# Optimization experiments

Hardware: AMD Instinct MI355X
Metric: run time of the kernel (lower is better)

## Reference

```python
import jax, jax.numpy as jnp
import numpy as np

H1, H, OUT, T = 512, 2048, 1024, 4096

def setup_inputs() -> dict:
    key = jax.random.key(0)
    ks = jax.random.split(key, 20)
    s = 0.02
    return {
        "input": jax.random.normal(ks[0], (1, OUT), jnp.float32),
        "hidden": jax.random.normal(ks[1], (1, 1, H), jnp.float32) * 0.1,
        "encoder_outputs": jax.random.normal(ks[2], (T, H), jnp.float32),
        "prenet_w": jax.random.normal(ks[3], (H1, OUT), jnp.float32) * s,
        "prenet_b": jnp.zeros((H1,), jnp.float32),
        "prenet2_w": jax.random.normal(ks[4], (H, H1), jnp.float32) * s,
        "prenet2_b": jnp.zeros((H,), jnp.float32),
        "attn1_w": jax.random.normal(ks[5], (H, H), jnp.float32) * s,
        "attn2_w": jax.random.normal(ks[6], (H, H), jnp.float32) * s,
        "attn3_w": jax.random.normal(ks[7], (1, H), jnp.float32) * s,
        "gru_w_ih": jax.random.normal(ks[8], (3 * H, 2 * H), jnp.float32) * s,
        "gru_w_hh": jax.random.normal(ks[9], (3 * H, H), jnp.float32) * s,
        "gru_b_ih": jnp.zeros((3 * H,), jnp.float32),
        "gru_b_hh": jnp.zeros((3 * H,), jnp.float32),
        "lin_w": jax.random.normal(ks[10], (OUT, H), jnp.float32) * s,
        "lin_b": jnp.zeros((OUT,), jnp.float32),
    }

def reference(input, hidden, encoder_outputs, prenet_w, prenet_b, prenet2_w,
              prenet2_b, attn1_w, attn2_w, attn3_w, gru_w_ih, gru_w_hh,
              gru_b_ih, gru_b_hh, lin_w, lin_b):
    # prenet MLP (dropout in eval mode = identity)
    em6 = jax.nn.relu(jax.nn.relu(input @ prenet_w.T + prenet_b) @ prenet2_w.T + prenet2_b)  # [1,H]
    # Bahdanau additive attention
    way = em6 @ attn1_w.T                                 # [1,H]
    uah = encoder_outputs @ attn2_w.T                     # [T,H]
    beta = jnp.tanh(way + uah)                            # [T,H] (broadcast = expand_as)
    gamma = beta @ attn3_w.T                              # [T,1]
    attn_weights = jax.nn.softmax(gamma.T, axis=1)        # [1,T]
    attn_applied = attn_weights @ encoder_outputs         # [1,H]
    # single-step GRU (PyTorch gate order: r, z, n)
    x = jnp.concatenate([em6, attn_applied], axis=1)      # [1,2H]
    h0 = hidden[0]                                        # [1,H]
    gi = x @ gru_w_ih.T + gru_b_ih                        # [1,3H]
    gh = h0 @ gru_w_hh.T + gru_b_hh                       # [1,3H]
    i_r, i_z, i_n = jnp.split(gi, 3, axis=1)
    h_r, h_z, h_n = jnp.split(gh, 3, axis=1)
    r = jax.nn.sigmoid(i_r + h_r)
    z = jax.nn.sigmoid(i_z + h_z)
    n = jnp.tanh(i_n + r * h_n)
    h_new = (1.0 - z) * n + z * h0                        # [1,H]
    out = jax.nn.softmax(h_new @ lin_w.T + lin_b, axis=1) # [1,OUT]
    return out, h_new[None], attn_weights
```

## Files before the change

### kernel.cpp

```cpp
#include <hip/hip_runtime.h>
#include <hip/hip_bf16.h>

typedef __bf16 bf16x8 __attribute__((ext_vector_type(8)));
typedef __bf16 bf16x4 __attribute__((ext_vector_type(4)));
typedef float f32x4 __attribute__((ext_vector_type(4)));

#define H1 512
#define H 2048
#define OUTN 1024
#define T 4096

__global__ __launch_bounds__(256) void matvec_k(
    const float* __restrict__ W, const float* __restrict__ x,
    const float* __restrict__ b, float* __restrict__ out,
    int R, int K, int relu)
{
    int row = blockIdx.x * 4 + (threadIdx.x >> 6);
    int lane = threadIdx.x & 63;
    if (row >= R) return;
    const float* Wr = W + (size_t)row * K;
    float s = 0.f;
    for (int k = lane * 4; k < K; k += 256) {
        float4 w4 = *(const float4*)(Wr + k);
        float4 x4 = *(const float4*)(x + k);
        s += w4.x * x4.x + w4.y * x4.y + w4.z * x4.z + w4.w * x4.w;
    }
    #pragma unroll
    for (int m = 32; m; m >>= 1) s += __shfl_xor(s, m, 64);
    if (lane == 0) {
        if (b) s += b[row];
        if (relu) s = fmaxf(s, 0.f);
        out[row] = s;
    }
}

__global__ __launch_bounds__(256) void cvt_frag_k(
    const float* __restrict__ E, const float* __restrict__ W2,
    __bf16* __restrict__ dst, float* __restrict__ zero_acc)
{
    if (blockIdx.x == 0) {
        #pragma unroll
        for (int j = 0; j < 8; ++j)
            zero_acc[threadIdx.x + 256 * j] = 0.f;
    }
    const int EC = T * H / 8;
    int c = blockIdx.x * 256 + threadIdx.x;
    const float* src;
    __bf16* d;
    if (c < EC) {
        int lane = c & 63;
        int k32 = (c >> 6) & 63;
        int r16 = c >> 12;
        int row = r16 * 16 + (lane & 15);
        int col = k32 * 32 + (lane >> 4) * 8;
        src = E + (size_t)row * H + col;
        d = dst + (size_t)c * 8;
    } else {
        int c2 = c - EC;
        int row = c2 >> 8;
        int kc = c2 & 255;
        src = W2 + (size_t)row * H + kc * 8;
        int grp = kc >> 3, cc = kc & 7;
        int sw = cc ^ (row & 7);
        d = dst + (size_t)T * H + (size_t)row * H + grp * 64 + sw * 8;
    }
    float4 a = *(const float4*)src;
    float4 b = *(const float4*)(src + 4);
    bf16x8 v = {(__bf16)a.x, (__bf16)a.y, (__bf16)a.z, (__bf16)a.w,
                (__bf16)b.x, (__bf16)b.y, (__bf16)b.z, (__bf16)b.w};
    *(bf16x8*)d = v;
}

__global__ __launch_bounds__(256, 4) void gamma_gemm8p(
    const __bf16* __restrict__ Efrag,
    const __bf16* __restrict__ Bsw,
    const float* __restrict__ way, const float* __restrict__ a3,
    float* __restrict__ gpart)
{
    __shared__ __attribute__((aligned(16))) __bf16 Bs[64][64];
    __shared__ float wayS[64], a3S[64];

    const int tb = blockIdx.x, hb = blockIdx.y;
    const int tid = threadIdx.x, lane = tid & 63, wid = tid >> 6;
    if (tid < 64) { wayS[tid] = way[hb * 64 + tid]; a3S[tid] = a3[hb * 64 + tid]; }

    const int K = 2048;
    const int rl = lane & 15;
    const int kg = (lane >> 4) * 8;
    const __bf16* Abase = Efrag + (((size_t)(tb * 8 + wid * 2) * 64) * 64 + lane) * 8;
    const __bf16* Bp = Bsw + (size_t)(hb * 64) * K;

    f32x4 acc[2][4] = {};

    for (int t = 0; t < 32; ++t) {
        const int k0 = t * 64;
        #pragma unroll
        for (int j = 0; j < 2; ++j) {
            int c = tid + j * 256;
            int row_ = c >> 3, cc_ = c & 7;
            const __bf16* s_ = Bp + (size_t)row_ * K + k0 + cc_ * 8;
            __builtin_amdgcn_global_load_lds(
                (const __attribute__((address_space(1))) void*)s_,
                (__attribute__((address_space(3))) void*)((char*)&Bs[0][0] + c * 16),
                16, 0, 0);
        }
        bf16x8 af[2][2];
        #pragma unroll
        for (int mi = 0; mi < 2; ++mi)
            #pragma unroll
            for (int kk = 0; kk < 2; ++kk)
                af[mi][kk] = *(const bf16x8*)(Abase +
                    ((size_t)(mi * 64 + t * 2 + kk) * 64) * 8);

        __syncthreads();

        #pragma unroll
        for (int kk = 0; kk < 2; ++kk) {
            bf16x8 bfm[4];
            const int kb = (kg + kk * 32) * 2;
            #pragma unroll
            for (int ni = 0; ni < 4; ++ni) {
                int r_ = ni * 16 + rl;
                bfm[ni] = *(const bf16x8*)((const char*)&Bs[0][0] + r_ * 128 + (kb ^ ((r_ & 7) << 4)));
            }
            #pragma unroll
            for (int mi = 0; mi < 2; ++mi)
                #pragma unroll
                for (int ni = 0; ni < 4; ++ni)
                    acc[mi][ni] = __builtin_amdgcn_mfma_f32_16x16x32_bf16(
                        af[mi][kk], bfm[ni], acc[mi][ni], 0, 0, 0);
        }
        __syncthreads();
    }

    const int rg = lane >> 4;
    #pragma unroll
    for (int mi = 0; mi < 2; ++mi) {
        float sr[4] = {0.f, 0.f, 0.f, 0.f};
        #pragma unroll
        for (int ni = 0; ni < 4; ++ni) {
            int h = ni * 16 + rl;
            float wh = wayS[h];
            float ah = a3S[h];
            #pragma unroll
            for (int r = 0; r < 4; ++r)
                sr[r] += tanhf(wh + acc[mi][ni][r]) * ah;
        }
        #pragma unroll
        for (int m = 1; m < 16; m <<= 1) {
            #pragma unroll
            for (int r = 0; r < 4; ++r)
                sr[r] += __shfl_xor(sr[r], m, 64);
        }
        if (rl == 0) {
            int t_ = tb * 128 + wid * 32 + mi * 16 + rg * 4;
            #pragma unroll
            for (int r = 0; r < 4; ++r)
                gpart[hb * T + t_ + r] = sr[r];
        }
    }
}

__global__ __launch_bounds__(256) void gsum_k(
    const float* __restrict__ gpart, float* __restrict__ gamma)
{
    int t = blockIdx.x * 256 + threadIdx.x;
    float s0 = 0.f, s1 = 0.f, s2 = 0.f, s3 = 0.f;
    #pragma unroll
    for (int hb = 0; hb < 32; hb += 4) {
        s0 += gpart[(hb + 0) * T + t];
        s1 += gpart[(hb + 1) * T + t];
        s2 += gpart[(hb + 2) * T + t];
        s3 += gpart[(hb + 3) * T + t];
    }
    gamma[t] = (s0 + s1) + (s2 + s3);
}

__global__ __launch_bounds__(1024) void softmax_k(
    const float* __restrict__ in, float* __restrict__ out, int n)
{
    __shared__ float sred[16];
    __shared__ float sbc;
    int tid = threadIdx.x;

    float m = -3.4e38f;
    for (int i = tid; i < n; i += 1024) m = fmaxf(m, in[i]);
    #pragma unroll
    for (int s = 32; s; s >>= 1) m = fmaxf(m, __shfl_xor(m, s, 64));
    if ((tid & 63) == 0) sred[tid >> 6] = m;
    __syncthreads();
    if (tid == 0) {
        float mm = sred[0];
        for (int i = 1; i < 16; ++i) mm = fmaxf(mm, sred[i]);
        sbc = mm;
    }
    __syncthreads();
    float mx = sbc;

    float s = 0.f;
    for (int i = tid; i < n; i += 1024) s += expf(in[i] - mx);
    #pragma unroll
    for (int sh = 32; sh; sh >>= 1) s += __shfl_xor(s, sh, 64);
    if ((tid & 63) == 0) sred[tid >> 6] = s;
    __syncthreads();
    if (tid == 0) {
        float ss = 0.f;
        for (int i = 0; i < 16; ++i) ss += sred[i];
        sbc = ss;
    }
    __syncthreads();
    float inv = 1.f / sbc;
    for (int i = tid; i < n; i += 1024) out[i] = expf(in[i] - mx) * inv;
}

__global__ __launch_bounds__(256) void attn_apply_k(
    const float* __restrict__ E, const float* __restrict__ w,
    float* __restrict__ outacc)
{
    int tid = threadIdx.x;
    int t0 = blockIdx.x * 32;
    float a[8] = {0.f, 0.f, 0.f, 0.f, 0.f, 0.f, 0.f, 0.f};
    for (int t = t0; t < t0 + 32; ++t) {
        float wt = w[t];
        const float* Er = E + (size_t)t * H;
        #pragma unroll
        for (int j = 0; j < 8; ++j)
            a[j] += wt * Er[tid + 256 * j];
    }
    #pragma unroll
    for (int j = 0; j < 8; ++j)
        atomicAdd(&outacc[tid + 256 * j], a[j]);
}

__global__ __launch_bounds__(256) void gru_combine_k(
    const float* __restrict__ gi, const float* __restrict__ gh,
    const float* __restrict__ h0, float* __restrict__ hout)
{
    int h = blockIdx.x * 256 + threadIdx.x;
    float ir = gi[h], iz = gi[H + h], in_ = gi[2 * H + h];
    float hr = gh[h], hz = gh[H + h], hn = gh[2 * H + h];
    float r = 1.f / (1.f + expf(-(ir + hr)));
    float z = 1.f / (1.f + expf(-(iz + hz)));
    float n = tanhf(in_ + r * hn);
    hout[h] = (1.f - z) * n + z * h0[h];
}

#define BM 128
#define BN 128
#define BK 32
#define LSTR 40

__global__ __launch_bounds__(256) void gamma_gemm(
    const float* __restrict__ E, const float* __restrict__ W2,
    const float* __restrict__ way, const float* __restrict__ a3,
    float* __restrict__ gamma)
{
    __shared__ __bf16 As[BM][LSTR];
    __shared__ __bf16 Bs[BN][LSTR];
    __shared__ float wayS[BN];
    __shared__ float a3S[BN];

    const int tb = blockIdx.x, hb = blockIdx.y;
    const int tid = threadIdx.x, lane = tid & 63, wid = tid >> 6;
    const int wr = wid >> 1, wc = wid & 1;
    if (tid < BN) { wayS[tid] = way[hb * BN + tid]; a3S[tid] = a3[hb * BN + tid]; }

    f32x4 acc[4][4] = {};
    const int K = 2048;
    const float* Ep  = E  + (size_t)(tb * BM) * K;
    const float* W2p = W2 + (size_t)(hb * BN) * K;
    const int rl = lane & 15;
    const int kg = (lane >> 4) * 8;

    for (int k0 = 0; k0 < K; k0 += BK) {
        __syncthreads();
        #pragma unroll
        for (int i = 0; i < 4; ++i) {
            int c = tid + i * 256;
            int row = c >> 3;
            int col = (c & 7) * 4;
            float4 va = *(const float4*)(Ep + (size_t)row * K + k0 + col);
            bf16x4 pa = {(__bf16)va.x, (__bf16)va.y, (__bf16)va.z, (__bf16)va.w};
            *(bf16x4*)&As[row][col] = pa;
            float4 vb = *(const float4*)(W2p + (size_t)row * K + k0 + col);
            bf16x4 pb = {(__bf16)vb.x, (__bf16)vb.y, (__bf16)vb.z, (__bf16)vb.w};
            *(bf16x4*)&Bs[row][col] = pb;
        }
        __syncthreads();
        bf16x8 af[4], bfr[4];
        #pragma unroll
        for (int mi = 0; mi < 4; ++mi)
            af[mi] = *(const bf16x8*)&As[wr * 64 + mi * 16 + rl][kg];
        #pragma unroll
        for (int ni = 0; ni < 4; ++ni)
            bfr[ni] = *(const bf16x8*)&Bs[wc * 64 + ni * 16 + rl][kg];
        #pragma unroll
        for (int mi = 0; mi < 4; ++mi)
            #pragma unroll
            for (int ni = 0; ni < 4; ++ni)
                acc[mi][ni] = __builtin_amdgcn_mfma_f32_16x16x32_bf16(
                    af[mi], bfr[ni], acc[mi][ni], 0, 0, 0);
    }

    const int rg = lane >> 4;
    #pragma unroll
    for (int mi = 0; mi < 4; ++mi) {
        float sr[4] = {0.f, 0.f, 0.f, 0.f};
        #pragma unroll
        for (int ni = 0; ni < 4; ++ni) {
            int h = wc * 64 + ni * 16 + rl;
            float wh = wayS[h];
            float ah = a3S[h];
            #pragma unroll
            for (int r = 0; r < 4; ++r)
                sr[r] += tanhf(wh + acc[mi][ni][r]) * ah;
        }
        #pragma unroll
        for (int m = 1; m < 16; m <<= 1) {
            #pragma unroll
            for (int r = 0; r < 4; ++r)
                sr[r] += __shfl_xor(sr[r], m, 64);
        }
        if (rl == 0) {
            int t = tb * BM + wr * 64 + mi * 16 + rg * 4;
            #pragma unroll
            for (int r = 0; r < 4; ++r)
                atomicAdd(&gamma[t + r], sr[r]);
        }
    }
}

extern "C" void kernel_launch(void* const* d_in, const int* in_sizes, int n_in,
                              void* d_out, int out_size, void* d_ws, size_t ws_size,
                              hipStream_t stream)
{
    const float* input    = (const float*)d_in[0];
    const float* hidden   = (const float*)d_in[1];
    const float* enc      = (const float*)d_in[2];
    const float* prenet_w = (const float*)d_in[3];
    const float* prenet_b = (const float*)d_in[4];
    const float* prenet2_w= (const float*)d_in[5];
    const float* prenet2_b= (const float*)d_in[6];
    const float* attn1_w  = (const float*)d_in[7];
    const float* attn2_w  = (const float*)d_in[8];
    const float* attn3_w  = (const float*)d_in[9];
    const float* gru_w_ih = (const float*)d_in[10];
    const float* gru_w_hh = (const float*)d_in[11];
    const float* gru_b_ih = (const float*)d_in[12];
    const float* gru_b_hh = (const float*)d_in[13];
    const float* lin_w    = (const float*)d_in[14];
    const float* lin_b    = (const float*)d_in[15];

    float* out = (float*)d_out;
    float* h_new = out + OUTN;
    float* attn_w = out + OUTN + H;

    float* ws = (float*)d_ws;
    float* w_h1     = ws;
    float* w_way    = w_h1 + 512;
    float* w_x      = w_way + H;
    float* w_logits = w_x + 2 * H;
    float* w_gamma  = w_logits + OUTN;
    float* w_gi     = w_gamma + T;
    float* w_gh     = w_gi + 3 * H;
    float* w_gpart  = w_gh + 3 * H;

    const size_t BF_OFF = 1 << 20;
    const size_t BF_BYTES = (size_t)(T + H) * H * sizeof(__bf16);
    bool fast = (ws_size >= BF_OFF + BF_BYTES);
    __bf16* bfE  = (__bf16*)((char*)d_ws + BF_OFF);
    __bf16* bfW2 = bfE + (size_t)T * H;

    if (fast) {
        cvt_frag_k<<<(T + H) * (H / 8) / 256, 256, 0, stream>>>(enc, attn2_w, bfE, w_x + H);
    } else {
        hipMemsetAsync(w_x + H, 0, H * sizeof(float), stream);
    }

    matvec_k<<<H1 / 4, 256, 0, stream>>>(prenet_w, input, prenet_b, w_h1, H1, OUTN, 1);
    matvec_k<<<H / 4, 256, 0, stream>>>(prenet2_w, w_h1, prenet2_b, w_x, H, H1, 1);
    matvec_k<<<H / 4, 256, 0, stream>>>(attn1_w, w_x, nullptr, w_way, H, H, 0);

    if (fast) {
        gamma_gemm8p<<<dim3(T / 128, H / 64), 256, 0, stream>>>(bfE, bfW2, w_way, attn3_w, w_gpart);
        gsum_k<<<T / 256, 256, 0, stream>>>(w_gpart, w_gamma);
        softmax_k<<<1, 1024, 0, stream>>>(w_gamma, attn_w, T);
    } else {
        hipMemsetAsync(w_gamma, 0, T * sizeof(float), stream);
        gamma_gemm<<<dim3(T / BM, H / BN), 256, 0, stream>>>(enc, attn2_w, w_way, attn3_w, w_gamma);
        softmax_k<<<1, 1024, 0, stream>>>(w_gamma, attn_w, T);
    }

    attn_apply_k<<<T / 32, 256, 0, stream>>>(enc, attn_w, w_x + H);
    matvec_k<<<(3 * H) / 4, 256, 0, stream>>>(gru_w_ih, w_x, gru_b_ih, w_gi, 3 * H, 2 * H, 0);
    matvec_k<<<(3 * H) / 4, 256, 0, stream>>>(gru_w_hh, hidden, gru_b_hh, w_gh, 3 * H, H, 0);
    gru_combine_k<<<H / 256, 256, 0, stream>>>(w_gi, w_gh, hidden, h_new);
    matvec_k<<<OUTN / 4, 256, 0, stream>>>(lin_w, h_new, lin_b, w_logits, OUTN, H, 0);
    softmax_k<<<1, 1024, 0, stream>>>(w_logits, out, OUTN);
}
```

Before: 121.1 us.

## Template matvec with unrolled dual accumulators; apply attention from bf16 fragments

Adds a templated matvec kernel with compile-time K, a fully unrolled loop and two accumulators, and uses it for all matvecs. The attention-apply step now reads the bf16 fragment copy of the encoder outputs that was already made for the gamma GEMM, instead of the fp32 original. This halves the bytes read for that step. It adds shuffle reductions over 16 lanes and uses bf16 precision for the weighted sum.

```diff
diff --git a/kernel.cpp b/kernel.cpp
--- a/kernel.cpp
+++ b/kernel.cpp
@@ -9,6 +9,33 @@
 #define H 2048
 #define OUTN 1024
 #define T 4096
+
+template<int K, bool RELU>
+__global__ __launch_bounds__(256) void matvec_t_k(
+    const float* __restrict__ W, const float* __restrict__ x,
+    const float* __restrict__ b, float* __restrict__ out)
+{
+    const int row = blockIdx.x * 4 + (threadIdx.x >> 6);
+    const int lane = threadIdx.x & 63;
+    const float* Wr = W + (size_t)row * K;
+    float s0 = 0.f, s1 = 0.f;
+    #pragma unroll
+    for (int i = 0; i < K / 256; ++i) {
+        int k = lane * 4 + i * 256;
+        float4 w4 = *(const float4*)(Wr + k);
+        float4 x4 = *(const float4*)(x + k);
+        if (i & 1) s1 += w4.x * x4.x + w4.y * x4.y + w4.z * x4.z + w4.w * x4.w;
+        else       s0 += w4.x * x4.x + w4.y * x4.y + w4.z * x4.z + w4.w * x4.w;
+    }
+    float s = s0 + s1;
+    #pragma unroll
+    for (int m = 32; m; m >>= 1) s += __shfl_xor(s, m, 64);
+    if (lane == 0) {
+        if (b) s += b[row];
+        if (RELU) s = fmaxf(s, 0.f);
+        out[row] = s;
+    }
+}
 
 __global__ __launch_bounds__(256) void matvec_k(
     const float* __restrict__ W, const float* __restrict__ x,
@@ -213,6 +240,36 @@
     for (int i = tid; i < n; i += 1024) out[i] = expf(in[i] - mx) * inv;
 }
 
+__global__ __launch_bounds__(256) void attn_apply_frag_k(
+    const __bf16* __restrict__ Efrag, const float* __restrict__ w,
+    float* __restrict__ outacc)
+{
+    const int wid = threadIdx.x >> 6, lane = threadIdx.x & 63;
+    const int k32 = blockIdx.x * 4 + wid;
+    const int r16b = blockIdx.y * 32;
+    const int tlow = lane & 15;
+    float a[8] = {0.f, 0.f, 0.f, 0.f, 0.f, 0.f, 0.f, 0.f};
+    for (int r16 = r16b; r16 < r16b + 32; ++r16) {
+        bf16x8 v = *(const bf16x8*)(Efrag + (((size_t)r16 * 64 + k32) * 64 + lane) * 8);
+        float wt = w[r16 * 16 + tlow];
+        #pragma unroll
+        for (int j = 0; j < 8; ++j)
+            a[j] += wt * (float)v[j];
+    }
+    #pragma unroll
+    for (int m = 1; m < 16; m <<= 1) {
+        #pragma unroll
+        for (int j = 0; j < 8; ++j)
+            a[j] += __shfl_xor(a[j], m, 64);
+    }
+    if (tlow == 0) {
+        int h = k32 * 32 + (lane >> 4) * 8;
+        #pragma unroll
+        for (int j = 0; j < 8; ++j)
+            atomicAdd(&outacc[h + j], a[j]);
+    }
+}
+
 __global__ __launch_bounds__(256) void attn_apply_k(
     const float* __restrict__ E, const float* __restrict__ w,
     float* __restrict__ outacc)
@@ -377,9 +434,9 @@
         hipMemsetAsync(w_x + H, 0, H * sizeof(float), stream);
     }
 
-    matvec_k<<<H1 / 4, 256, 0, stream>>>(prenet_w, input, prenet_b, w_h1, H1, OUTN, 1);
-    matvec_k<<<H / 4, 256, 0, stream>>>(prenet2_w, w_h1, prenet2_b, w_x, H, H1, 1);
-    matvec_k<<<H / 4, 256, 0, stream>>>(attn1_w, w_x, nullptr, w_way, H, H, 0);
+    matvec_t_k<OUTN, true><<<H1 / 4, 256, 0, stream>>>(prenet_w, input, prenet_b, w_h1);
+    matvec_t_k<H1, true><<<H / 4, 256, 0, stream>>>(prenet2_w, w_h1, prenet2_b, w_x);
+    matvec_t_k<H, false><<<H / 4, 256, 0, stream>>>(attn1_w, w_x, nullptr, w_way);
 
     if (fast) {
         gamma_gemm8p<<<dim3(T / 128, H / 64), 256, 0, stream>>>(bfE, bfW2, w_way, attn3_w, w_gpart);
@@ -391,10 +448,14 @@
         softmax_k<<<1, 1024, 0, stream>>>(w_gamma, attn_w, T);
     }
 
-    attn_apply_k<<<T / 32, 256, 0, stream>>>(enc, attn_w, w_x + H);
-    matvec_k<<<(3 * H) / 4, 256, 0, stream>>>(gru_w_ih, w_x, gru_b_ih, w_gi, 3 * H, 2 * H, 0);
-    matvec_k<<<(3 * H) / 4, 256, 0, stream>>>(gru_w_hh, hidden, gru_b_hh, w_gh, 3 * H, H, 0);
+    if (fast)
+        attn_apply_frag_k<<<dim3(16, 8), 256, 0, stream>>>(bfE, attn_w, w_x + H);
+    else
+        attn_apply_k<<<T / 32, 256, 0, stream>>>(enc, attn_w, w_x + H);
+
+    matvec_t_k<2 * H, false><<<(3 * H) / 4, 256, 0, stream>>>(gru_w_ih, w_x, gru_b_ih, w_gi);
+    matvec_t_k<H, false><<<(3 * H) / 4, 256, 0, stream>>>(gru_w_hh, hidden, gru_b_hh, w_gh);
     gru_combine_k<<<H / 256, 256, 0, stream>>>(w_gi, w_gh, hidden, h_new);
-    matvec_k<<<OUTN / 4, 256, 0, stream>>>(lin_w, h_new, lin_b, w_logits, OUTN, H, 0);
+    matvec_t_k<H, false><<<OUTN / 4, 256, 0, stream>>>(lin_w, h_new, lin_b, w_logits);
     softmax_k<<<1, 1024, 0, stream>>>(w_logits, out, OUTN);
 }
```

Measured after the change: 114.5 us, median of 2. -5.5%, faster.
